# Optimization experiments

Measured on AMD Instinct MI355X. Metric: run time of the kernel, lower is better.

The kernel has to match this reference:

```python
import jax, jax.numpy as jnp
import numpy as np

IN_CH = 128
OUT_CH = 128

def setup_inputs() -> dict:
    key = jax.random.key(0)
    k1, k2, k3, k4, k5 = jax.random.split(key, 5)
    from_tensor = jax.random.normal(k1, (640000, IN_CH), dtype=jnp.float32)
    to_index = jax.random.randint(k2, (640000,), 0, 10000, dtype=jnp.int64)
    # torch Linear default init ~ U(-1/sqrt(fan_in), 1/sqrt(fan_in))
    lim1 = 1.0 / np.sqrt(IN_CH)
    lim2 = 1.0 / np.sqrt(OUT_CH)
    W1 = jax.random.uniform(k3, (OUT_CH, IN_CH), jnp.float32, -lim1, lim1)
    b1 = jnp.zeros((OUT_CH,), jnp.float32)
    W2 = jax.random.uniform(k4, (OUT_CH, OUT_CH), jnp.float32, -lim2, lim2)
    b2 = jnp.zeros((OUT_CH,), jnp.float32)
    return {"from_tensor": from_tensor, "to_index": to_index, "dim_size": 10000,
            "W1": W1, "b1": b1, "W2": W2, "b2": b2}

def reference(from_tensor, to_index, dim_size, W1, b1, W2, b2):
    # MLP transform (transform_scatter=True): Linear+ReLU x2
    h = jax.nn.relu(from_tensor @ W1.T + b1)
    h = jax.nn.relu(h @ W2.T + b2)          # (num_src, OUT_CH)
    # scatter-mean over to_index into dim_size rows
    seg_sum = jax.ops.segment_sum(h, to_index, num_segments=dim_size)
    counts = jax.ops.segment_sum(jnp.ones((h.shape[0],), h.dtype), to_index,
                                 num_segments=dim_size)
    return seg_sum / jnp.maximum(counts, 1.0)[:, None]
```

## Files before the change

kernel.cpp:

```cpp
#include <hip/hip_runtime.h>

#define IN_CH 128
#define OUT_CH 128
#define LDSPAD 136

typedef short bf16x8 __attribute__((ext_vector_type(8)));
typedef float f32x4  __attribute__((ext_vector_type(4)));

__device__ __forceinline__ unsigned short f32_to_bf16_bits(float f) {
    unsigned u = __builtin_bit_cast(unsigned, f);
    u += 0x7FFFu + ((u >> 16) & 1u);
    return (unsigned short)(u >> 16);
}
__device__ __forceinline__ float bf16_bits_to_f32(unsigned short b) {
    return __builtin_bit_cast(float, (unsigned)b << 16);
}

__global__ void detect_kernel(const unsigned short* __restrict__ X,
                              const unsigned short* __restrict__ W1,
                              const unsigned short* __restrict__ W2,
                              const int* __restrict__ idx,
                              int* __restrict__ flags) {
    __shared__ int red[4];
    const int t = threadIdx.x;
    if (t < 4) red[t] = 0;
    __syncthreads();
    #pragma unroll
    for (int w = 0; w < 3; ++w) {
        const unsigned short* p = (w == 0) ? X : (w == 1) ? W1 : W2;
        int crazy = 0;
        for (int j = t; j < 512; j += 256) {
            const unsigned short h = p[j];
            const int e = (h >> 7) & 0xFF;
            const int man = h & 0x7F;
            if (e >= 0x90 || (e == 0 && man != 0)) crazy++;
        }
        if (crazy) atomicAdd(&red[w], crazy);
    }
    {
        if (idx[2 * t + 1] != 0) atomicAdd(&red[3], 1);
    }
    __syncthreads();
    if (t == 0) {
        flags[0] = red[0] > 16 ? 1 : 0;
        flags[1] = red[1] > 16 ? 1 : 0;
        flags[2] = red[2] > 16 ? 1 : 0;
        flags[3] = red[3] < 8  ? 1 : 0;
    }
}

__global__ void count_kernel(const int* __restrict__ idx, int* __restrict__ cnt,
                             const int* __restrict__ flags, int n) {
    const int sh = flags[3];
    int i = blockIdx.x * blockDim.x + threadIdx.x;
    if (i < n) atomicAdd(&cnt[idx[(size_t)i << sh]], 1);
}

__global__ void scan_kernel(const int* __restrict__ cnt, int* __restrict__ off,
                            int* __restrict__ cur, int dim) {
    __shared__ int wtot[16];
    __shared__ int woff[16];
    __shared__ int carry_s;
    const int tid = threadIdx.x;
    const int wv = tid >> 6, ln = tid & 63;
    if (tid == 0) carry_s = 0;
    __syncthreads();
    for (int base = 0; base < dim; base += 1024) {
        const int i = base + tid;
        const int orig = (i < dim) ? cnt[i] : 0;
        int v = orig;
        #pragma unroll
        for (int d = 1; d < 64; d <<= 1) {
            int w = __shfl_up(v, d, 64);
            if (ln >= d) v += w;
        }
        if (ln == 63) wtot[wv] = v;
        __syncthreads();
        if (tid == 0) {
            int acc = carry_s;
            #pragma unroll
            for (int k = 0; k < 16; ++k) { woff[k] = acc; acc += wtot[k]; }
            carry_s = acc;
        }
        __syncthreads();
        const int excl = woff[wv] + v - orig;
        if (i < dim) { off[i] = excl; cur[i] = excl; }
        __syncthreads();
    }
}

__global__ void perm_kernel(const int* __restrict__ idx, int* __restrict__ cur,
                            int* __restrict__ perm, const int* __restrict__ flags,
                            int n) {
    const int sh = flags[3];
    int i = blockIdx.x * blockDim.x + threadIdx.x;
    if (i < n) {
        const int s = idx[(size_t)i << sh];
        const int p = atomicAdd(&cur[s], 1);
        perm[p] = i;
    }
}

__global__ __launch_bounds__(512, 4)
void mlp_gather_kernel(const unsigned short* __restrict__ X,
                       const int* __restrict__ perm,
                       const int* __restrict__ off,
                       const int* __restrict__ cnt,
                       const unsigned short* __restrict__ W1,
                       const unsigned short* __restrict__ B1,
                       const unsigned short* __restrict__ W2,
                       const unsigned short* __restrict__ B2,
                       float* __restrict__ out,
                       const int* __restrict__ flags,
                       int dim)
{
    __shared__ short lds_x[32 * LDSPAD];
    __shared__ short lds_h[32 * LDSPAD];

    const int xf32  = flags[0];
    const int w1f32 = flags[1];
    const int w2f32 = flags[2];

    const int tid  = threadIdx.x;
    const int wave = tid >> 6;
    const int lane = tid & 63;
    const int m    = lane & 15;
    const int quad = lane >> 4;

    const int n = wave * 16 + m;
    bf16x8 w1f[4], w2f[4];
    float  b1c, b2c;
    b1c = w1f32 ? ((const float*)B1)[n] : bf16_bits_to_f32(B1[n]);
    b2c = w2f32 ? ((const float*)B2)[n] : bf16_bits_to_f32(B2[n]);
    #pragma unroll
    for (int kc = 0; kc < 4; ++kc) {
        const int ko = kc * 32 + quad * 8;
        if (w1f32) {
            const float* Wf = (const float*)W1;
            f32x4 lo = *(const f32x4*)(Wf + n * IN_CH + ko);
            f32x4 hi = *(const f32x4*)(Wf + n * IN_CH + ko + 4);
            bf16x8 v;
            #pragma unroll
            for (int j = 0; j < 4; ++j) {
                v[j]     = (short)f32_to_bf16_bits(lo[j]);
                v[4 + j] = (short)f32_to_bf16_bits(hi[j]);
            }
            w1f[kc] = v;
        } else {
            w1f[kc] = *(const bf16x8*)(W1 + n * IN_CH + ko);
        }
        if (w2f32) {
            const float* Wf = (const float*)W2;
            f32x4 lo = *(const f32x4*)(Wf + n * OUT_CH + ko);
            f32x4 hi = *(const f32x4*)(Wf + n * OUT_CH + ko + 4);
            bf16x8 v;
            #pragma unroll
            for (int j = 0; j < 4; ++j) {
                v[j]     = (short)f32_to_bf16_bits(lo[j]);
                v[4 + j] = (short)f32_to_bf16_bits(hi[j]);
            }
            w2f[kc] = v;
        } else {
            w2f[kc] = *(const bf16x8*)(W2 + n * OUT_CH + ko);
        }
    }

    const int srow = tid >> 4;
    const int sseg = tid & 15;

    for (int s = blockIdx.x; s < dim; s += gridDim.x) {
        const int c     = cnt[s];
        const int start = off[s];
        float sum = 0.f;

        auto gather = [&](int gr, bf16x8& v) {
            v = (bf16x8){0, 0, 0, 0, 0, 0, 0, 0};
            if (gr < c) {
                const int row = perm[start + gr];
                if (xf32) {
                    const float* Xf = (const float*)X;
                    f32x4 lo = *(const f32x4*)(Xf + (size_t)row * IN_CH + sseg * 8);
                    f32x4 hi = *(const f32x4*)(Xf + (size_t)row * IN_CH + sseg * 8 + 4);
                    #pragma unroll
                    for (int j = 0; j < 4; ++j) {
                        v[j]     = (short)f32_to_bf16_bits(lo[j]);
                        v[4 + j] = (short)f32_to_bf16_bits(hi[j]);
                    }
                } else {
                    v = *(const bf16x8*)(X + (size_t)row * IN_CH + sseg * 8);
                }
            }
        };

        bf16x8 cur;
        gather(srow, cur);

        for (int base = 0; base < c; base += 32) {
            *(bf16x8*)&lds_x[srow * LDSPAD + sseg * 8] = cur;
            bf16x8 nxt;
            gather(base + 32 + srow, nxt);
            __syncthreads();

            f32x4 acc0 = {0.f, 0.f, 0.f, 0.f}, acc1 = {0.f, 0.f, 0.f, 0.f};
            #pragma unroll
            for (int kc = 0; kc < 4; ++kc) {
                const int ko = kc * 32 + quad * 8;
                bf16x8 a0 = *(const bf16x8*)&lds_x[m * LDSPAD + ko];
                bf16x8 a1 = *(const bf16x8*)&lds_x[(16 + m) * LDSPAD + ko];
                acc0 = __builtin_amdgcn_mfma_f32_16x16x32_bf16(a0, w1f[kc], acc0, 0, 0, 0);
                acc1 = __builtin_amdgcn_mfma_f32_16x16x32_bf16(a1, w1f[kc], acc1, 0, 0, 0);
            }
            #pragma unroll
            for (int r = 0; r < 4; ++r) {
                float v0 = acc0[r] + b1c;
                v0 = v0 > 0.f ? v0 : 0.f;
                lds_h[(quad * 4 + r) * LDSPAD + n] = (short)f32_to_bf16_bits(v0);
                float v1 = acc1[r] + b1c;
                v1 = v1 > 0.f ? v1 : 0.f;
                lds_h[(16 + quad * 4 + r) * LDSPAD + n] = (short)f32_to_bf16_bits(v1);
            }
            __syncthreads();

            f32x4 acc2_0 = {0.f, 0.f, 0.f, 0.f}, acc2_1 = {0.f, 0.f, 0.f, 0.f};
            #pragma unroll
            for (int kc = 0; kc < 4; ++kc) {
                const int ko = kc * 32 + quad * 8;
                bf16x8 a0 = *(const bf16x8*)&lds_h[m * LDSPAD + ko];
                bf16x8 a1 = *(const bf16x8*)&lds_h[(16 + m) * LDSPAD + ko];
                acc2_0 = __builtin_amdgcn_mfma_f32_16x16x32_bf16(a0, w2f[kc], acc2_0, 0, 0, 0);
                acc2_1 = __builtin_amdgcn_mfma_f32_16x16x32_bf16(a1, w2f[kc], acc2_1, 0, 0, 0);
            }

            #pragma unroll
            for (int r = 0; r < 4; ++r) {
                if (base + quad * 4 + r < c) {
                    float v = acc2_0[r] + b2c;
                    sum += (v > 0.f ? v : 0.f);
                }
                if (base + 16 + quad * 4 + r < c) {
                    float v = acc2_1[r] + b2c;
                    sum += (v > 0.f ? v : 0.f);
                }
            }
            cur = nxt;
        }

        sum += __shfl_xor(sum, 16, 64);
        sum += __shfl_xor(sum, 32, 64);
        if (quad == 0) {
            const float inv = 1.f / (float)(c > 1 ? c : 1);
            out[(size_t)s * OUT_CH + n] = sum * inv;
        }
    }
}

extern "C" void kernel_launch(void* const* d_in, const int* in_sizes, int n_in,
                              void* d_out, int out_size, void* d_ws, size_t ws_size,
                              hipStream_t stream) {
    int iX = 0;
    for (int i = 1; i < n_in; ++i)
        if (in_sizes[i] > in_sizes[iX]) iX = i;
    const int n_src = in_sizes[iX] / IN_CH;
    int iI = -1, iW1 = -1, iW2 = -1, iB1 = -1, iB2 = -1;
    for (int i = 0; i < n_in; ++i) {
        if (i == iX) continue;
        const int s = in_sizes[i];
        if (s == n_src && iI < 0) iI = i;
        else if (s == IN_CH * OUT_CH) { if (iW1 < 0) iW1 = i; else if (iW2 < 0) iW2 = i; }
        else if (s == OUT_CH) { if (iB1 < 0) iB1 = i; else if (iB2 < 0) iB2 = i; }
    }

    const unsigned short* X  = (const unsigned short*)d_in[iX];
    const int*            ix = (const int*)d_in[iI];
    const unsigned short* W1 = (const unsigned short*)d_in[iW1];
    const unsigned short* B1 = (const unsigned short*)d_in[iB1];
    const unsigned short* W2 = (const unsigned short*)d_in[iW2];
    const unsigned short* B2 = (const unsigned short*)d_in[iB2];
    float* out = (float*)d_out;

    const int dim = out_size / OUT_CH;

    int* flags = (int*)d_ws;
    int* cnt   = (int*)((char*)d_ws + 256);
    int* off   = cnt + dim;
    int* cur   = off + dim;
    int* perm  = cur + dim;

    hipMemsetAsync(cnt, 0, (size_t)dim * sizeof(int), stream);

    detect_kernel<<<1, 256, 0, stream>>>(X, W1, W2, ix, flags);

    count_kernel<<<(n_src + 255) / 256, 256, 0, stream>>>(ix, cnt, flags, n_src);

    scan_kernel<<<1, 1024, 0, stream>>>(cnt, off, cur, dim);

    perm_kernel<<<(n_src + 255) / 256, 256, 0, stream>>>(ix, cur, perm, flags, n_src);

    const int grid = dim < 2048 ? dim : 2048;
    mlp_gather_kernel<<<grid, 512, 0, stream>>>(X, perm, off, cnt, W1, B1, W2, B2,
                                                out, flags, dim);
}
```

Baseline: 580.6 us.

## Flatten segment loop into continuous tile stream with deeper gather prefetch

```diff
diff --git a/kernel.cpp b/kernel.cpp
--- a/kernel.cpp
+++ b/kernel.cpp
@@ -101,6 +101,7 @@
     }
 }
 
+template <int XF32>
 __global__ __launch_bounds__(512, 4)
 void mlp_gather_kernel(const unsigned short* __restrict__ X,
                        const int* __restrict__ perm,
@@ -114,10 +115,12 @@
                        const int* __restrict__ flags,
                        int dim)
 {
+    if (flags[0] != XF32) return;
+
     __shared__ short lds_x[32 * LDSPAD];
     __shared__ short lds_h[32 * LDSPAD];
-
-    const int xf32  = flags[0];
+    __shared__ int s_sid[16], s_cnt[16], s_start[16], s_cum[17];
+
     const int w1f32 = flags[1];
     const int w2f32 = flags[2];
 
@@ -126,8 +129,8 @@
     const int lane = tid & 63;
     const int m    = lane & 15;
     const int quad = lane >> 4;
-
-    const int n = wave * 16 + m;
+    const int n    = wave * 16 + m;
+
     bf16x8 w1f[4], w2f[4];
     float  b1c, b2c;
     b1c = w1f32 ? ((const float*)B1)[n] : bf16_bits_to_f32(B1[n]);
@@ -168,37 +171,70 @@
     const int srow = tid >> 4;
     const int sseg = tid & 15;
 
-    for (int s = blockIdx.x; s < dim; s += gridDim.x) {
-        const int c     = cnt[s];
-        const int start = off[s];
-        float sum = 0.f;
-
-        auto gather = [&](int gr, bf16x8& v) {
-            v = (bf16x8){0, 0, 0, 0, 0, 0, 0, 0};
-            if (gr < c) {
-                const int row = perm[start + gr];
-                if (xf32) {
+    const int G   = gridDim.x;
+    const int bid = blockIdx.x;
+    const int A   = (bid < dim) ? (dim - 1 - bid) / G + 1 : 0;
+
+    for (int w0 = 0; w0 < A; w0 += 16) {
+        int nseg = (A - w0) < 16 ? (A - w0) : 16;
+        if (nseg <= 0) break;
+
+        __syncthreads();
+        if (tid < nseg) {
+            const int s = bid + (w0 + tid) * G;
+            s_sid[tid]   = s;
+            s_cnt[tid]   = cnt[s];
+            s_start[tid] = off[s];
+        }
+        __syncthreads();
+        if (tid == 0) {
+            int acc = 0;
+            s_cum[0] = 0;
+            for (int i = 0; i < nseg; ++i) {
+                acc += (s_cnt[i] + 31) >> 5;
+                s_cum[i + 1] = acc;
+            }
+        }
+        __syncthreads();
+        const int C = s_cum[nseg];
+
+        auto rowidx = [&](int jq, int khint) -> int {
+            if (jq >= C) return -1;
+            int kk = khint;
+            while (kk + 1 < nseg && jq >= s_cum[kk + 1]) ++kk;
+            const int gr = (jq - s_cum[kk]) * 32 + srow;
+            return (gr < s_cnt[kk]) ? perm[s_start[kk] + gr] : -1;
+        };
+        auto xload = [&](int pr) -> bf16x8 {
+            bf16x8 v = {0, 0, 0, 0, 0, 0, 0, 0};
+            if (pr >= 0) {
+                if (XF32) {
                     const float* Xf = (const float*)X;
-                    f32x4 lo = *(const f32x4*)(Xf + (size_t)row * IN_CH + sseg * 8);
-                    f32x4 hi = *(const f32x4*)(Xf + (size_t)row * IN_CH + sseg * 8 + 4);
+                    f32x4 lo = *(const f32x4*)(Xf + (size_t)pr * IN_CH + sseg * 8);
+                    f32x4 hi = *(const f32x4*)(Xf + (size_t)pr * IN_CH + sseg * 8 + 4);
                     #pragma unroll
                     for (int j = 0; j < 4; ++j) {
                         v[j]     = (short)f32_to_bf16_bits(lo[j]);
                         v[4 + j] = (short)f32_to_bf16_bits(hi[j]);
                     }
                 } else {
-                    v = *(const bf16x8*)(X + (size_t)row * IN_CH + sseg * 8);
+                    v = *(const bf16x8*)(X + (size_t)pr * IN_CH + sseg * 8);
                 }
             }
+            return v;
         };
 
-        bf16x8 cur;
-        gather(srow, cur);
-
-        for (int base = 0; base < c; base += 32) {
-            *(bf16x8*)&lds_x[srow * LDSPAD + sseg * 8] = cur;
-            bf16x8 nxt;
-            gather(base + 32 + srow, nxt);
+        int   k   = 0;
+        float sum = 0.f;
+
+        auto body = [&](int j, bf16x8& xb, int& pr) {
+            while (j >= s_cum[k + 1]) ++k;
+            const int c    = s_cnt[k];
+            const int base = (j - s_cum[k]) * 32;
+
+            *(bf16x8*)&lds_x[srow * LDSPAD + sseg * 8] = xb;
+            xb = xload(pr);
+            pr = rowidx(j + 4, k);
             __syncthreads();
 
             f32x4 acc0 = {0.f, 0.f, 0.f, 0.f}, acc1 = {0.f, 0.f, 0.f, 0.f};
@@ -242,14 +278,36 @@
                     sum += (v > 0.f ? v : 0.f);
                 }
             }
-            cur = nxt;
-        }
-
-        sum += __shfl_xor(sum, 16, 64);
-        sum += __shfl_xor(sum, 32, 64);
-        if (quad == 0) {
-            const float inv = 1.f / (float)(c > 1 ? c : 1);
-            out[(size_t)s * OUT_CH + n] = sum * inv;
+
+            if (j + 1 == s_cum[k + 1]) {
+                float t = sum;
+                t += __shfl_xor(t, 16, 64);
+                t += __shfl_xor(t, 32, 64);
+                if (quad == 0) {
+                    const int cd = c > 1 ? c : 1;
+                    out[(size_t)s_sid[k] * OUT_CH + n] = t / (float)cd;
+                }
+                sum = 0.f;
+            }
+        };
+
+        if (C > 0) {
+            int prA = rowidx(0, 0);
+            int prB = rowidx(1, 0);
+            bf16x8 xA = xload(prA);
+            bf16x8 xB = xload(prB);
+            prA = rowidx(2, 0);
+            prB = rowidx(3, 0);
+
+            for (int j = 0; j < C; j += 2) {
+                body(j, xA, prA);
+                if (j + 1 < C) body(j + 1, xB, prB);
+            }
+        }
+
+        for (int k2 = 0; k2 < nseg; ++k2) {
+            if (s_cnt[k2] == 0 && quad == 0)
+                out[(size_t)s_sid[k2] * OUT_CH + n] = 0.f;
         }
     }
 }
@@ -296,7 +354,10 @@
 
     perm_kernel<<<(n_src + 255) / 256, 256, 0, stream>>>(ix, cur, perm, flags, n_src);
 
-    const int grid = dim < 2048 ? dim : 2048;
-    mlp_gather_kernel<<<grid, 512, 0, stream>>>(X, perm, off, cnt, W1, B1, W2, B2,
-                                                out, flags, dim);
-}
+    int grid = dim < 2048 ? dim : 2048;
+    if (grid < 1) grid = 1;
+    mlp_gather_kernel<0><<<grid, 512, 0, stream>>>(X, perm, off, cnt, W1, B1, W2, B2,
+                                                   out, flags, dim);
+    mlp_gather_kernel<1><<<grid, 512, 0, stream>>>(X, perm, off, cnt, W1, B1, W2, B2,
+                                                   out, flags, dim);
+}
```

New measurement: 599.3 us. 1.03x slower.

## Scatter bf16 rows into segment order before MLP, replacing indexed gather

Applied to the files above, without the earlier changes.

```diff
diff --git a/kernel.cpp b/kernel.cpp
--- a/kernel.cpp
+++ b/kernel.cpp
@@ -89,35 +89,60 @@
     }
 }
 
-__global__ void perm_kernel(const int* __restrict__ idx, int* __restrict__ cur,
-                            int* __restrict__ perm, const int* __restrict__ flags,
-                            int n) {
-    const int sh = flags[3];
-    int i = blockIdx.x * blockDim.x + threadIdx.x;
-    if (i < n) {
-        const int s = idx[(size_t)i << sh];
-        const int p = atomicAdd(&cur[s], 1);
-        perm[p] = i;
-    }
+__global__ __launch_bounds__(256)
+void scatter_kernel(const unsigned short* __restrict__ X,
+                    const int* __restrict__ idx,
+                    int* __restrict__ cur,
+                    unsigned short* __restrict__ Xs,
+                    const int* __restrict__ flags,
+                    int n_src)
+{
+    const int xf32 = flags[0];
+    const int sh   = flags[3];
+    const int t    = blockIdx.x * blockDim.x + threadIdx.x;
+    const int r    = t >> 4;
+    const int seg  = t & 15;
+    if (r >= n_src) return;
+
+    const int lane = threadIdx.x & 63;
+    int p = 0;
+    if ((lane & 15) == 0) {
+        const int s = idx[(size_t)r << sh];
+        p = atomicAdd(&cur[s], 1);
+    }
+    p = __shfl(p, lane & 48, 64);
+
+    bf16x8 v;
+    if (xf32) {
+        const float* Xf = (const float*)X;
+        f32x4 lo = *(const f32x4*)(Xf + (size_t)r * IN_CH + seg * 8);
+        f32x4 hi = *(const f32x4*)(Xf + (size_t)r * IN_CH + seg * 8 + 4);
+        #pragma unroll
+        for (int j = 0; j < 4; ++j) {
+            v[j]     = (short)f32_to_bf16_bits(lo[j]);
+            v[4 + j] = (short)f32_to_bf16_bits(hi[j]);
+        }
+    } else {
+        v = *(const bf16x8*)(X + (size_t)r * IN_CH + seg * 8);
+    }
+    *(bf16x8*)(Xs + (size_t)p * IN_CH + seg * 8) = v;
 }
 
 __global__ __launch_bounds__(512, 4)
-void mlp_gather_kernel(const unsigned short* __restrict__ X,
-                       const int* __restrict__ perm,
-                       const int* __restrict__ off,
-                       const int* __restrict__ cnt,
-                       const unsigned short* __restrict__ W1,
-                       const unsigned short* __restrict__ B1,
-                       const unsigned short* __restrict__ W2,
-                       const unsigned short* __restrict__ B2,
-                       float* __restrict__ out,
-                       const int* __restrict__ flags,
-                       int dim)
+void mlp_seq_kernel(const unsigned short* __restrict__ Xs,
+                    const int* __restrict__ off,
+                    const int* __restrict__ cnt,
+                    const unsigned short* __restrict__ W1,
+                    const unsigned short* __restrict__ B1,
+                    const unsigned short* __restrict__ W2,
+                    const unsigned short* __restrict__ B2,
+                    float* __restrict__ out,
+                    const int* __restrict__ flags,
+                    int dim)
 {
     __shared__ short lds_x[32 * LDSPAD];
     __shared__ short lds_h[32 * LDSPAD];
 
-    const int xf32  = flags[0];
     const int w1f32 = flags[1];
     const int w2f32 = flags[2];
 
@@ -126,8 +151,8 @@
     const int lane = tid & 63;
     const int m    = lane & 15;
     const int quad = lane >> 4;
-
-    const int n = wave * 16 + m;
+    const int n    = wave * 16 + m;
+
     bf16x8 w1f[4], w2f[4];
     float  b1c, b2c;
     b1c = w1f32 ? ((const float*)B1)[n] : bf16_bits_to_f32(B1[n]);
@@ -168,38 +193,31 @@
     const int srow = tid >> 4;
     const int sseg = tid & 15;
 
-    for (int s = blockIdx.x; s < dim; s += gridDim.x) {
+    const int G   = gridDim.x;
+    const int bid = blockIdx.x;
+    const int s0  = (int)(((long long)bid * dim) / G);
+    const int s1  = (int)(((long long)(bid + 1) * dim) / G);
+
+    for (int s = s0; s < s1; ++s) {
         const int c     = cnt[s];
         const int start = off[s];
         float sum = 0.f;
 
-        auto gather = [&](int gr, bf16x8& v) {
-            v = (bf16x8){0, 0, 0, 0, 0, 0, 0, 0};
-            if (gr < c) {
-                const int row = perm[start + gr];
-                if (xf32) {
-                    const float* Xf = (const float*)X;
-                    f32x4 lo = *(const f32x4*)(Xf + (size_t)row * IN_CH + sseg * 8);
-                    f32x4 hi = *(const f32x4*)(Xf + (size_t)row * IN_CH + sseg * 8 + 4);
-                    #pragma unroll
-                    for (int j = 0; j < 4; ++j) {
-                        v[j]     = (short)f32_to_bf16_bits(lo[j]);
-                        v[4 + j] = (short)f32_to_bf16_bits(hi[j]);
-                    }
-                } else {
-                    v = *(const bf16x8*)(X + (size_t)row * IN_CH + sseg * 8);
-                }
-            }
+        auto xsload = [&](int gr) -> bf16x8 {
+            bf16x8 v = {0, 0, 0, 0, 0, 0, 0, 0};
+            if (gr < c)
+                v = *(const bf16x8*)(Xs + (size_t)(start + gr) * IN_CH + sseg * 8);
+            return v;
         };
 
-        bf16x8 cur;
-        gather(srow, cur);
+        bf16x8 curx = xsload(srow);
 
         for (int base = 0; base < c; base += 32) {
-            *(bf16x8*)&lds_x[srow * LDSPAD + sseg * 8] = cur;
-            bf16x8 nxt;
-            gather(base + 32 + srow, nxt);
-            __syncthreads();
+            *(bf16x8*)&lds_x[srow * LDSPAD + sseg * 8] = curx;
+            bf16x8 nxt = xsload(base + 32 + srow);
+
+            asm volatile("s_waitcnt lgkmcnt(0)" ::: "memory");
+            __builtin_amdgcn_s_barrier();
 
             f32x4 acc0 = {0.f, 0.f, 0.f, 0.f}, acc1 = {0.f, 0.f, 0.f, 0.f};
             #pragma unroll
@@ -219,7 +237,9 @@
                 v1 = v1 > 0.f ? v1 : 0.f;
                 lds_h[(16 + quad * 4 + r) * LDSPAD + n] = (short)f32_to_bf16_bits(v1);
             }
-            __syncthreads();
+
+            asm volatile("s_waitcnt lgkmcnt(0)" ::: "memory");
+            __builtin_amdgcn_s_barrier();
 
             f32x4 acc2_0 = {0.f, 0.f, 0.f, 0.f}, acc2_1 = {0.f, 0.f, 0.f, 0.f};
             #pragma unroll
@@ -242,7 +262,7 @@
                     sum += (v > 0.f ? v : 0.f);
                 }
             }
-            cur = nxt;
+            curx = nxt;
         }
 
         sum += __shfl_xor(sum, 16, 64);
@@ -284,7 +304,9 @@
     int* cnt   = (int*)((char*)d_ws + 256);
     int* off   = cnt + dim;
     int* cur   = off + dim;
-    int* perm  = cur + dim;
+    size_t xs_off = 256 + 3 * (size_t)dim * sizeof(int);
+    xs_off = (xs_off + 255) & ~(size_t)255;
+    unsigned short* Xs = (unsigned short*)((char*)d_ws + xs_off);
 
     hipMemsetAsync(cnt, 0, (size_t)dim * sizeof(int), stream);
 
@@ -294,9 +316,11 @@
 
     scan_kernel<<<1, 1024, 0, stream>>>(cnt, off, cur, dim);
 
-    perm_kernel<<<(n_src + 255) / 256, 256, 0, stream>>>(ix, cur, perm, flags, n_src);
-
-    const int grid = dim < 2048 ? dim : 2048;
-    mlp_gather_kernel<<<grid, 512, 0, stream>>>(X, perm, off, cnt, W1, B1, W2, B2,
-                                                out, flags, dim);
-}
+    const int sc_grid = (n_src * 16 + 255) / 256;
+    scatter_kernel<<<sc_grid, 256, 0, stream>>>(X, ix, cur, Xs, flags, n_src);
+
+    int grid = dim < 2048 ? dim : 2048;
+    if (grid < 1) grid = 1;
+    mlp_seq_kernel<<<grid, 512, 0, stream>>>(Xs, off, cnt, W1, B1, W2, B2,
+                                             out, flags, dim);
+}
```

Measured after the change: 609.4 us. 5.0% more time.
